# Kernel optimization log

Measured on AMD Instinct MI355X. Metric: run time of the kernel, lower is better.

Reference implementation:

```python
import jax, jax.numpy as jnp
import numpy as np

DIM = 192
HEADS = 4
HID = int(DIM * 2.66)  # 510, Restormer GDFN hidden dim
EPS_LN = 1e-6


def ln2d(x, w, b):
    # torch LayerNorm2d variant: global mean/std over (C,H,W), std is UNBIASED (ddof=1)
    n = x.shape[1] * x.shape[2] * x.shape[3]
    mean = x.mean(axis=(1, 2, 3), keepdims=True)
    var = ((x - mean) ** 2).sum(axis=(1, 2, 3), keepdims=True) / (n - 1)
    return (x - mean) / (jnp.sqrt(var) + EPS_LN) * w + b


def conv1x1(x, w):
    # w: [O, C]; pointwise conv as channel matmul
    return jnp.einsum('bchw,oc->bohw', x, w)


def dwconv3(x, w):
    # w: [C, 1, 3, 3] depthwise 3x3, padding=1
    return jax.lax.conv_general_dilated(
        x, w, window_strides=(1, 1), padding='SAME',
        dimension_numbers=('NCHW', 'OIHW', 'NCHW'),
        feature_group_count=x.shape[1])


def setup_inputs() -> dict:
    key = jax.random.key(0)
    ks = jax.random.split(key, 8)
    s = 0.02
    return {
        'x': jax.random.normal(ks[0], (2, DIM, 256, 256), dtype=jnp.float32),
        'n1_w': jnp.ones((1, DIM, 1, 1), jnp.float32),
        'n1_b': jnp.zeros((1, DIM, 1, 1), jnp.float32),
        'qkv_w': jax.random.normal(ks[1], (3 * DIM, DIM), jnp.float32) * s,
        'qkv_dw_w': jax.random.normal(ks[2], (3 * DIM, 1, 3, 3), jnp.float32) * s,
        'proj_w': jax.random.normal(ks[3], (DIM, DIM), jnp.float32) * s,
        'temperature': jnp.ones((HEADS, 1, 1), jnp.float32),
        'n2_w': jnp.ones((1, DIM, 1, 1), jnp.float32),
        'n2_b': jnp.zeros((1, DIM, 1, 1), jnp.float32),
        'ff_in_w': jax.random.normal(ks[4], (2 * HID, DIM), jnp.float32) * s,
        'ff_dw_w': jax.random.normal(ks[5], (2 * HID, 1, 3, 3), jnp.float32) * s,
        'ff_out_w': jax.random.normal(ks[6], (DIM, HID), jnp.float32) * s,
    }


def reference(x, n1_w, n1_b, qkv_w, qkv_dw_w, proj_w, temperature,
              n2_w, n2_b, ff_in_w, ff_dw_w, ff_out_w):
    b, c, h, w = x.shape
    hd = c // HEADS

    # ---- MDTA attention ----
    y = ln2d(x, n1_w, n1_b)
    qkv = dwconv3(conv1x1(y, qkv_w), qkv_dw_w)  # [b, 3c, h, w]
    q, k, v = jnp.split(qkv, 3, axis=1)
    q = q.reshape(b, HEADS, hd, h * w)
    k = k.reshape(b, HEADS, hd, h * w)
    v = v.reshape(b, HEADS, hd, h * w)
    # L2-normalize along spatial axis (F.normalize, eps=1e-12)
    q = q / jnp.maximum(jnp.linalg.norm(q, axis=-1, keepdims=True), 1e-12)
    k = k / jnp.maximum(jnp.linalg.norm(k, axis=-1, keepdims=True), 1e-12)
    attn = jnp.einsum('bhcn,bhdn->bhcd', q, k) * temperature  # [b,H,hd,hd]
    attn = jax.nn.softmax(attn, axis=-1)
    out = jnp.einsum('bhcd,bhdn->bhcn', attn, v).reshape(b, c, h, w)
    x = x + conv1x1(out, proj_w)

    # ---- GDFN feed-forward ----
    y = ln2d(x, n2_w, n2_b)
    y = dwconv3(conv1x1(y, ff_in_w), ff_dw_w)  # [b, 2*HID, h, w]
    x1, x2 = jnp.split(y, 2, axis=1)
    y = jax.nn.gelu(x1, approximate=False) * x2
    x = x + conv1x1(y, ff_out_w)
    return x
```

## Files before the change

### kernel.cpp

```cpp
#include <hip/hip_runtime.h>
#include <hip/hip_bf16.h>

typedef unsigned short u16;
typedef __attribute__((ext_vector_type(8))) short short8;
typedef __attribute__((ext_vector_type(8))) unsigned short ushort8v;
typedef __attribute__((ext_vector_type(4))) float f32x4;

#define NPIX  65536
#define HH    256
#define WW    256
#define BATCH 2
#define CDIM  192
#define NHEADS 4
#define HD    48
#define OQKV  576
#define HIDN  510
#define OPAD  1024
#define NSLOT 32

__device__ __forceinline__ float bf2f(u16 b) {
  union { unsigned u; float f; } v; v.u = ((unsigned)b) << 16; return v.f;
}
__device__ __forceinline__ u16 f2bf(float f) {
  __bf16 h = (__bf16)f;
  u16 r; __builtin_memcpy(&r, &h, 2); return r;
}
__device__ __forceinline__ void atomAddF(float* p, float v) { unsafeAtomicAdd(p, v); }
__device__ __forceinline__ void gload16(const void* g, void* l) {
  __builtin_amdgcn_global_load_lds((const __attribute__((address_space(1))) unsigned int*)g,
                                   (__attribute__((address_space(3))) unsigned int*)l, 16, 0, 0);
}
__device__ __forceinline__ void xcdswz(int& bx, int& by) {
  const int nx = gridDim.x;
  const int tot = nx * gridDim.y;
  const int lin = by * nx + bx;
  const int q = tot >> 3, r = tot & 7;
  const int xcd = lin & 7, pos = lin >> 3;
  const int nl = (xcd < r) ? (xcd * (q + 1) + pos) : (r * (q + 1) + (xcd - r) * q + pos);
  bx = nl % nx; by = nl / nx;
}
__device__ __forceinline__ void dw3row(const u16* __restrict__ rp, int jm, bool hasL, bool hasR,
                                       float w0, float w1, float w2, float* acc) {
  ushort8v m = *(const ushort8v*)(rp + jm);
  float f[10];
  f[0] = hasL ? bf2f(rp[jm - 1]) : 0.f;
  #pragma unroll
  for (int t = 0; t < 8; ++t) f[t + 1] = bf2f(m[t]);
  f[9] = hasR ? bf2f(rp[jm + 8]) : 0.f;
  #pragma unroll
  for (int i = 0; i < 8; ++i) acc[i] += w0 * f[i] + w1 * f[i + 1] + w2 * f[i + 2];
}

#define OFF_STATS1 ((size_t)0)
#define OFF_STATS2 ((size_t)512)
#define OFF_G      ((size_t)1024)
#define OFF_NQ     (OFF_G + 2359296)
#define OFF_NK     (OFF_NQ + 49152)
#define ZERO_BYTES (OFF_NK + 49152)
#define OFF_BQ     ZERO_BYTES
#define OFF_B2     (OFF_BQ + 4608)
#define OFF_M      (OFF_B2 + 8192)
#define OFF_WQ     (OFF_M + 294912)
#define OFF_W2B    (OFF_WQ + 442368)
#define OFF_W3     (OFF_W2B + 786432)
#define OFF_T      (OFF_W3 + 196608)
#define OFF_QKV    (OFF_T + 50331648)
#define OFF_BAND   (OFF_QKV + 150994944)

__global__ __launch_bounds__(256) void k_statsT(const float* __restrict__ P, u16* __restrict__ T,
                                                float* __restrict__ stats) {
  __shared__ u16 ld[128][200];
  const int b = blockIdx.y, n0 = blockIdx.x * 128, tid = threadIdx.x;
  const int slot = blockIdx.x & (NSLOT - 1);
  const float* Pb = P + (((size_t)b * CDIM) << 16) + n0;
  float s = 0.f, ss = 0.f;
  for (int it = 0; it < 24; ++it) {
    int idx = it * 256 + tid;
    int c = idx >> 5, j = idx & 31;
    float4 v = *(const float4*)(Pb + ((size_t)c << 16) + j * 4);
    s  += v.x + v.y + v.z + v.w;
    ss += v.x*v.x + v.y*v.y + v.z*v.z + v.w*v.w;
    int px = j * 4;
    ld[px][c] = f2bf(v.x); ld[px+1][c] = f2bf(v.y);
    ld[px+2][c] = f2bf(v.z); ld[px+3][c] = f2bf(v.w);
  }
  for (int off = 32; off; off >>= 1) { s += __shfl_down(s, off); ss += __shfl_down(ss, off); }
  __shared__ float ls[4], lss[4];
  const int wid = tid >> 6, lane = tid & 63;
  if (lane == 0) { ls[wid] = s; lss[wid] = ss; }
  __syncthreads();
  if (tid == 0) {
    atomAddF(&stats[(slot * BATCH + b) * 2 + 0], ls[0]+ls[1]+ls[2]+ls[3]);
    atomAddF(&stats[(slot * BATCH + b) * 2 + 1], lss[0]+lss[1]+lss[2]+lss[3]);
  }
  u16* Tb = T + (size_t)(b * NPIX + n0) * CDIM;
  for (int it = 0; it < 12; ++it) {
    int idx = it * 256 + tid;
    int ch = idx % 24, nl = idx / 24;
    union { u16 s[8]; uint4 v; } t;
    #pragma unroll
    for (int r = 0; r < 8; ++r) t.s[r] = ld[nl][ch * 8 + r];
    int sch = ch ^ (nl & 7);
    *(uint4*)((char*)(Tb + (size_t)nl * CDIM) + sch * 16) = t.v;
  }
}

__global__ void k_fold(const float* __restrict__ w_in, const float* __restrict__ ln_w,
                       const float* __restrict__ ln_b, const float* __restrict__ stats,
                       u16* __restrict__ W, float* __restrict__ bias, int O_real) {
  const int o = blockIdx.x, b = blockIdx.y, c = threadIdx.x;
  const int Mtot = gridDim.x;
  const float n = (float)(CDIM * NPIX);
  float sum = 0.f, sumsq = 0.f;
  for (int sl = 0; sl < NSLOT; ++sl) {
    sum   += stats[(sl * BATCH + b) * 2 + 0];
    sumsq += stats[(sl * BATCH + b) * 2 + 1];
  }
  const float mean = sum / n;
  const float var = (sumsq - sum * sum / n) / (n - 1.f);
  const float inv = 1.f / (sqrtf(var) + 1e-6f);
  float we = 0.f, cb = 0.f;
  if (o < O_real) {
    float wi = w_in[o * CDIM + c];
    float a  = ln_w[c] * inv;
    we = wi * a;
    cb = wi * (ln_b[c] - mean * a);
  }
  int sch = (c >> 3) ^ (o & 7);
  W[((size_t)b * Mtot + o) * CDIM + sch * 8 + (c & 7)] = f2bf(we);
  for (int off = 32; off; off >>= 1) cb += __shfl_down(cb, off);
  __shared__ float l[3];
  if ((threadIdx.x & 63) == 0) l[threadIdx.x >> 6] = cb;
  __syncthreads();
  if (threadIdx.x == 0) bias[b * Mtot + o] = l[0] + l[1] + l[2];
}

__global__ void k_fold3(const float* __restrict__ w, u16* __restrict__ W3) {
  const int o = blockIdx.x;
  for (int it = 0; it < 2; ++it) {
    int c = it * 256 + threadIdx.x;
    float v = (c < HIDN) ? w[o * HIDN + c] : 0.f;
    int sch = (c >> 3) ^ (o & 7);
    W3[o * 512 + sch * 8 + (c & 7)] = f2bf(v);
  }
}

template <int KTOT, int KC, int EPI, int STATS, int NT>
__global__ __launch_bounds__(256) void k_mgemm(
    const u16* __restrict__ Bm, const u16* __restrict__ Am,
    const float* __restrict__ bias,
    const u16* __restrict__ rT, long rTbstr,
    void* __restrict__ outv, long Obstr, int out_nstr,
    u16* __restrict__ tout, long toutbstr,
    int Mtot, long Bbstr, long Abstr,
    int nB_base, int nB_rows, int nO_base, float* __restrict__ stats)
{
  constexpr int RBC = KC * 2;
  constexpr int NFR = NT / 64;
  constexpr int LDSB = (NT + 64) * KC * 2;
  constexpr int EPIB = (EPI == 0) ? 64 * (NT + 8) * 2
                     : (EPI == 2) ? 128 * 66 * 4
                     : ((EPI == 3) ? 64 * 132 * 4 : 0);
  constexpr int TOT  = LDSB > EPIB ? LDSB : EPIB;
  __shared__ char lds[TOT];
  u16* lB = (u16*)lds;
  u16* lA = (u16*)(lds + NT * KC * 2);
  const int b = blockIdx.z;
  int bx = blockIdx.x, by = blockIdx.y;
  xcdswz(bx, by);
  const int o0 = bx * 64;
  const int nB = nB_base + by * NT;
  const int nO = nO_base + by * NT;
  const int tid = threadIdx.x;
  const int lane = tid & 63;
  const int wid = tid >> 6;

  if (EPI == 0 && (nB < 0 || nB >= nB_rows)) {
    u16* op = (u16*)outv;
    uint4 z; z.x = z.y = z.z = z.w = 0u;
    constexpr int CH8 = NT / 8;
    #pragma unroll
    for (int it = 0; it < NT / 32; ++it) {
      int idx = it * 256 + tid;
      int orow = idx / CH8, c8 = idx % CH8;
      *(uint4*)(op + (size_t)b * Obstr + (size_t)(o0 + orow) * out_nstr + nO + c8 * 8) = z;
    }
    return;
  }

  const u16* Bb = Bm + (size_t)b * Bbstr + (size_t)nB * KTOT;
  const u16* Ab = Am + (size_t)b * Abstr + (size_t)o0 * KTOT;

  f32x4 acc[4][NFR];
  #pragma unroll
  for (int m = 0; m < 4; ++m)
    #pragma unroll
    for (int nf = 0; nf < NFR; ++nf) acc[m][nf] = (f32x4){0.f, 0.f, 0.f, 0.f};

  for (int kc0 = 0; kc0 < KTOT; kc0 += KC) {
    if (kc0) __syncthreads();
    constexpr int NCH = KC / 8;
    #pragma unroll
    for (int it = 0; it < NT * NCH / 256; ++it) {
      int idx = it * 256 + tid; int r = idx / NCH, ch = idx % NCH;
      gload16((const char*)(Bb + (size_t)r * KTOT + kc0) + ch * 16, (char*)lB + idx * 16);
    }
    #pragma unroll
    for (int it = 0; it < 64 * NCH / 256; ++it) {
      int idx = it * 256 + tid; int r = idx / NCH, ch = idx % NCH;
      gload16((const char*)(Ab + (size_t)r * KTOT + kc0) + ch * 16, (char*)lA + idx * 16);
    }
    __syncthreads();
    const int lr = lane & 15, g = lane >> 4;
    #pragma unroll
    for (int ks = 0; ks < KC / 32; ++ks) {
      const int ck = ks * 4 + g;
      short8 afr[4], bfr[NFR];
      #pragma unroll
      for (int m = 0; m < 4; ++m) {
        int row = m * 16 + lr;
        afr[m] = *(const short8*)((const char*)lA + row * RBC + ((ck ^ (row & 7)) << 4));
      }
      #pragma unroll
      for (int nf = 0; nf < NFR; ++nf) {
        int row = wid * (NT / 4) + nf * 16 + lr;
        bfr[nf] = *(const short8*)((const char*)lB + row * RBC + ((ck ^ (row & 7)) << 4));
      }
      #pragma unroll
      for (int m = 0; m < 4; ++m)
        #pragma unroll
        for (int nf = 0; nf < NFR; ++nf)
          acc[m][nf] = __builtin_amdgcn_mfma_f32_16x16x32_bf16(afr[m], bfr[nf], acc[m][nf], 0, 0, 0);
    }
  }

  const int col = lane & 15, rg = lane >> 4;
  if constexpr (EPI == 0) {
    constexpr int NTP = NT + 8;
    u16* lst = (u16*)lds;
    __syncthreads();
    #pragma unroll
    for (int m = 0; m < 4; ++m)
      #pragma unroll
      for (int j = 0; j < 4; ++j) {
        int r = m * 16 + rg * 4 + j;
        float bv = bias[b * Mtot + o0 + r];
        #pragma unroll
        for (int nf = 0; nf < NFR; ++nf) {
          int nn = wid * (NT / 4) + nf * 16 + col;
          lst[r * NTP + nn] = f2bf(acc[m][nf][j] + bv);
        }
      }
    __syncthreads();
    u16* op = (u16*)outv;
    constexpr int CH8 = NT / 8;
    #pragma unroll
    for (int it = 0; it < 64 * CH8 / 256; ++it) {
      int idx = it * 256 + tid;
      int r = idx / CH8, ch = idx % CH8;
      uint4 v = *(const uint4*)(lst + r * NTP + ch * 8);
      *(uint4*)(op + (size_t)b * Obstr + (size_t)(o0 + r) * out_nstr + nO + ch * 8) = v;
    }
  } else if constexpr (EPI == 2) {
    float* lBf = (float*)lds;
    __syncthreads();
    #pragma unroll
    for (int m = 0; m < 4; ++m)
      #pragma unroll
      for (int nf = 0; nf < NFR; ++nf)
        #pragma unroll
        for (int j = 0; j < 4; ++j)
          lBf[(wid * 32 + nf * 16 + col) * 66 + m * 16 + rg * 4 + j] = acc[m][nf][j];
    __syncthreads();
    float s = 0.f, ss = 0.f;
    for (int it = 0; it < 4; ++it) {
      int idx = it * 256 + tid;
      int n = idx >> 3, ch3 = idx & 7;
      size_t rowoff = (size_t)(nO + n) * CDIM;
      int chunk = (o0 >> 3) + (ch3 ^ (n & 7));
      uint4 xv = *(const uint4*)((const char*)(rT + (size_t)b * rTbstr + rowoff) + chunk * 16);
      u16* xs = (u16*)&xv;
      union { u16 s[8]; uint4 v; } t;
      #pragma unroll
      for (int r = 0; r < 8; ++r) {
        float rv = bf2f(xs[r]) + lBf[n * 66 + ch3 * 8 + r];
        t.s[r] = f2bf(rv);
        if constexpr (STATS) { s += rv; ss += rv * rv; }
      }
      *(uint4*)((char*)(tout + (size_t)b * toutbstr + rowoff) + chunk * 16) = t.v;
    }
    if constexpr (STATS) {
      for (int off = 32; off; off >>= 1) { s += __shfl_down(s, off); ss += __shfl_down(ss, off); }
      __shared__ float sr1[4], sr2[4];
      if (lane == 0) { sr1[wid] = s; sr2[wid] = ss; }
      __syncthreads();
      if (tid == 0) {
        int slot = by & (NSLOT - 1);
        atomAddF(&stats[(slot * BATCH + b) * 2 + 0], sr1[0]+sr1[1]+sr1[2]+sr1[3]);
        atomAddF(&stats[(slot * BATCH + b) * 2 + 1], sr2[0]+sr2[1]+sr2[2]+sr2[3]);
      }
    }
  } else {
    u16* lAx = (u16*)lds;
    __syncthreads();
    for (int it = 0; it < 4; ++it) {
      int idx = it * 256 + tid;
      int n = idx >> 3, ch3 = idx & 7;
      int chunk = (o0 >> 3) + (ch3 ^ (n & 7));
      uint4 xv = *(const uint4*)((const char*)(rT + (size_t)b * rTbstr + (size_t)(nO + n) * CDIM) + chunk * 16);
      u16* xs = (u16*)&xv;
      #pragma unroll
      for (int r = 0; r < 8; ++r) lAx[n * 66 + ch3 * 8 + r] = xs[r];
    }
    __syncthreads();
    #pragma unroll
    for (int m = 0; m < 4; ++m)
      #pragma unroll
      for (int nf = 0; nf < NFR; ++nf)
        #pragma unroll
        for (int j = 0; j < 4; ++j) {
          int nl = wid * 32 + nf * 16 + col;
          acc[m][nf][j] += bf2f(lAx[nl * 66 + m * 16 + rg * 4 + j]);
        }
    __syncthreads();
    float* lstf = (float*)lds;
    #pragma unroll
    for (int m = 0; m < 4; ++m)
      #pragma unroll
      for (int nf = 0; nf < NFR; ++nf)
        #pragma unroll
        for (int j = 0; j < 4; ++j)
          lstf[(m * 16 + rg * 4 + j) * 132 + wid * 32 + nf * 16 + col] = acc[m][nf][j];
    __syncthreads();
    float* of = (float*)outv;
    #pragma unroll
    for (int it = 0; it < 8; ++it) {
      int idx = it * 256 + tid;
      int r = idx >> 5, q4 = idx & 31;
      float4 v = *(const float4*)&lstf[r * 132 + q4 * 4];
      *(float4*)(of + (size_t)b * Obstr + (size_t)(o0 + r) * out_nstr + nO + q4 * 4) = v;
    }
  }
}

__global__ __launch_bounds__(256) void k_gram(const u16* __restrict__ qkv,
                                              const float* __restrict__ dww,
                                              float* __restrict__ G,
                                              float* __restrict__ nq,
                                              float* __restrict__ nk) {
  __shared__ u16 qs[HD][128], ks2[HD][128];
  __shared__ u16 wq[HD][9], wk[HD][9];
  __shared__ float nql[HD], nkl[HD];
  int bx = blockIdx.x, by = blockIdx.y;
  xcdswz(bx, by);
  const int b = by >> 2, h = by & 3;
  const int row = bx >> 1, col0 = (bx & 1) * 128;
  const int slot = bx & (NSLOT - 1);
  const int bh = b * NHEADS + h;
  const int tid = threadIdx.x;

  for (int idx = tid; idx < HD * 9; idx += 256) {
    int c = idx / 9, k9 = idx % 9;
    wq[c][k9] = f2bf(dww[(h * HD + c) * 9 + k9]);
    wk[c][k9] = f2bf(dww[(CDIM + h * HD + c) * 9 + k9]);
  }
  __syncthreads();

  for (int it = 0; it < 6; ++it) {
    int idx = it * 256 + tid;
    int j = idx & 15, cz = idx >> 4;
    int c = cz % HD, qk = cz / HD;
    const u16* base = qkv + (((size_t)(b * OQKV + qk * CDIM + h * HD + c)) << 16);
    const u16* w = qk ? wk[c] : wq[c];
    float acc[8] = {0.f,0.f,0.f,0.f,0.f,0.f,0.f,0.f};
    const int jm = col0 + j * 8;
    const bool hasL = jm > 0, hasR = jm < 248;
    if (row > 0)   dw3row(base + (row - 1) * 256, jm, hasL, hasR, bf2f(w[0]), bf2f(w[1]), bf2f(w[2]), acc);
                   dw3row(base + row * 256,       jm, hasL, hasR, bf2f(w[3]), bf2f(w[4]), bf2f(w[5]), acc);
    if (row < 255) dw3row(base + (row + 1) * 256, jm, hasL, hasR, bf2f(w[6]), bf2f(w[7]), bf2f(w[8]), acc);
    union { u16 s[8]; ushort8v v; } rv;
    float sqs = 0.f;
    #pragma unroll
    for (int i = 0; i < 8; ++i) {
      rv.s[i] = f2bf(acc[i]);
      sqs += acc[i] * acc[i];
    }
    const int sw = (j ^ (c & 7)) * 8;
    if (qk) *(ushort8v*)&ks2[c][sw] = rv.v;
    else    *(ushort8v*)&qs[c][sw]  = rv.v;
    sqs += __shfl_down(sqs, 8);
    sqs += __shfl_down(sqs, 4);
    sqs += __shfl_down(sqs, 2);
    sqs += __shfl_down(sqs, 1);
    if ((tid & 15) == 0) { if (qk) nkl[c] = sqs; else nql[c] = sqs; }
  }
  __syncthreads();

  if (tid < HD) atomAddF(&nq[(slot * 2 * NHEADS + bh) * HD + tid], nql[tid]);
  else if (tid < 2*HD) atomAddF(&nk[(slot * 2 * NHEADS + bh) * HD + tid - HD], nkl[tid - HD]);

  const int lane = tid & 63, wid = tid >> 6;
  const int lr = lane & 15, g = lane >> 4;
  float* Gb = G + (size_t)(slot * 2 * NHEADS + bh) * HD * HD;
  for (int t = wid; t < 9; t += 4) {
    const int m = t / 3, nb = t % 3;
    f32x4 a4 = (f32x4){0.f, 0.f, 0.f, 0.f};
    #pragma unroll
    for (int ksi = 0; ksi < 4; ++ksi) {
      int ck = ksi * 4 + g;
      int ra = m * 16 + lr, rb = nb * 16 + lr;
      short8 af = *(const short8*)&qs[ra][(ck ^ (ra & 7)) * 8];
      short8 bf = *(const short8*)&ks2[rb][(ck ^ (rb & 7)) * 8];
      a4 = __builtin_amdgcn_mfma_f32_16x16x32_bf16(af, bf, a4, 0, 0, 0);
    }
    #pragma unroll
    for (int jj = 0; jj < 4; ++jj)
      atomAddF(&Gb[(m * 16 + g * 4 + jj) * HD + nb * 16 + lr], a4[jj]);
  }
}

__global__ void k_attnM(const float* __restrict__ G, const float* __restrict__ nq,
                        const float* __restrict__ nk, const float* __restrict__ temp,
                        const float* __restrict__ proj_w, u16* __restrict__ Mb16) {
  const int h = blockIdx.x, b = blockIdx.y;
  const int bh = b * NHEADS + h;
  __shared__ float at[HD][HD];
  __shared__ float nqs[HD], nks[HD];
  const int tid = threadIdx.x;
  if (tid < HD) {
    float s = 0.f;
    for (int sl = 0; sl < NSLOT; ++sl) s += nq[(sl * 2 * NHEADS + bh) * HD + tid];
    nqs[tid] = fmaxf(sqrtf(s), 1e-12f);
  } else if (tid >= 64 && tid < 64 + HD) {
    int c = tid - 64;
    float s = 0.f;
    for (int sl = 0; sl < NSLOT; ++sl) s += nk[(sl * 2 * NHEADS + bh) * HD + c];
    nks[c] = fmaxf(sqrtf(s), 1e-12f);
  }
  __syncthreads();
  const float t = temp[h];
  for (int idx = tid; idx < HD * HD; idx += 256) {
    int c = idx / HD, d = idx % HD;
    float g = 0.f;
    for (int sl = 0; sl < NSLOT; ++sl)
      g += G[(size_t)(sl * 2 * NHEADS + bh) * HD * HD + idx];
    at[c][d] = g / (nqs[c] * nks[d]) * t;
  }
  __syncthreads();
  if (tid < HD) {
    float m = -1e30f;
    for (int d = 0; d < HD; ++d) m = fmaxf(m, at[tid][d]);
    float s = 0.f;
    for (int d = 0; d < HD; ++d) { float e = __expf(at[tid][d] - m); at[tid][d] = e; s += e; }
    float inv = 1.f / s;
    for (int d = 0; d < HD; ++d) at[tid][d] *= inv;
  }
  __syncthreads();
  for (int idx = tid; idx < CDIM * HD; idx += 256) {
    int o = idx / HD, d = idx % HD;
    float acc = 0.f;
    for (int c = 0; c < HD; ++c) acc += proj_w[o * CDIM + h * HD + c] * at[c][d];
    int cf = h * HD + d;
    int sch = (cf >> 3) ^ (o & 7);
    Mb16[((size_t)(b * CDIM + o)) * CDIM + sch * 8 + (cf & 7)] = f2bf(acc);
  }
}

__global__ __launch_bounds__(256) void k_dwT(const u16* __restrict__ qkv,
                                             const float* __restrict__ dww,
                                             u16* __restrict__ vdwT, long vdwbstr) {
  __shared__ u16 ld[64][201];
  __shared__ float w9[CDIM][9];
  int bx = blockIdx.x, by = blockIdx.y;
  xcdswz(bx, by);
  const int b = by;
  const int p0 = bx * 64;
  const int row = p0 >> 8, col0 = p0 & 255;
  const int tid = threadIdx.x;
  for (int idx = tid; idx < CDIM * 9; idx += 256) w9[idx / 9][idx % 9] = dww[384 * 9 + idx];
  __syncthreads();
  for (int it = 0; it < 6; ++it) {
    int idx = it * 256 + tid;
    int j = idx & 7, c = idx >> 3;
    const u16* base = qkv + (((size_t)(b * OQKV + 384 + c)) << 16);
    const float* w = w9[c];
    float acc[8] = {0.f,0.f,0.f,0.f,0.f,0.f,0.f,0.f};
    const int jm = col0 + j * 8;
    const bool hasL = jm > 0, hasR = jm < 248;
    if (row > 0)   dw3row(base + (row - 1) * 256, jm, hasL, hasR, w[0], w[1], w[2], acc);
                   dw3row(base + row * 256,       jm, hasL, hasR, w[3], w[4], w[5], acc);
    if (row < 255) dw3row(base + (row + 1) * 256, jm, hasL, hasR, w[6], w[7], w[8], acc);
    #pragma unroll
    for (int i = 0; i < 8; ++i) ld[j * 8 + i][c] = f2bf(acc[i]);
  }
  __syncthreads();
  u16* Tb = vdwT + (size_t)b * vdwbstr + (size_t)p0 * CDIM;
  for (int it = 0; it < 6; ++it) {
    int idx = it * 256 + tid;
    int ch = idx % 24, pl = idx / 24;
    union { u16 s[8]; uint4 v; } t;
    #pragma unroll
    for (int r = 0; r < 8; ++r) t.s[r] = ld[pl][ch * 8 + r];
    int sch = ch ^ (pl & 7);
    *(uint4*)((char*)(Tb + (size_t)pl * CDIM) + sch * 16) = t.v;
  }
}

__global__ __launch_bounds__(256) void k_dwgT(const u16* __restrict__ hp_, const float* __restrict__ w9,
                                              u16* __restrict__ ygT, int rows_loc, int band_px) {
  __shared__ u16 ld[32][515];
  int bx = blockIdx.x, by = blockIdx.y;
  xcdswz(bx, by);
  const int b = by;
  const int p0 = bx * 32;
  const int olr = p0 >> 8, col0 = p0 & 255;
  const int tid = threadIdx.x;
  if (tid < 64) {
    int px = tid >> 1, c = 510 + (tid & 1);
    ld[px][c] = 0;
  }
  __syncthreads();
  for (int it = 0; it < 8; ++it) {
    int idx = it * 256 + tid;
    if (idx >= HIDN * 4) break;
    int j = idx & 3, c = idx >> 2;
    const u16* ia = hp_ + (size_t)(b * OPAD + c) * rows_loc * 256;
    const u16* ig = hp_ + (size_t)(b * OPAD + c + HIDN) * rows_loc * 256;
    float aa[8] = {0.f,0.f,0.f,0.f,0.f,0.f,0.f,0.f};
    float gg[8] = {0.f,0.f,0.f,0.f,0.f,0.f,0.f,0.f};
    const int jm = col0 + j * 8;
    const bool hasL = jm > 0, hasR = jm < 248;
    #pragma unroll
    for (int dr = 0; dr < 3; ++dr) {
      dw3row(ia + (olr + dr) * 256, jm, hasL, hasR,
             w9[c * 9 + dr * 3], w9[c * 9 + dr * 3 + 1], w9[c * 9 + dr * 3 + 2], aa);
      dw3row(ig + (olr + dr) * 256, jm, hasL, hasR,
             w9[(c + HIDN) * 9 + dr * 3], w9[(c + HIDN) * 9 + dr * 3 + 1],
             w9[(c + HIDN) * 9 + dr * 3 + 2], gg);
    }
    #pragma unroll
    for (int i = 0; i < 8; ++i) {
      float a = aa[i];
      float gel = 0.5f * a * (1.f + erff(a * 0.70710678118654752f));
      ld[j * 8 + i][c] = f2bf(gel * gg[i]);
    }
  }
  __syncthreads();
  u16* Tb = ygT + ((size_t)b * band_px + p0) * 512;
  for (int it = 0; it < 8; ++it) {
    int idx = it * 256 + tid;
    int ch = idx & 63, pl = idx >> 6;
    union { u16 s[8]; uint4 v; } t;
    #pragma unroll
    for (int r = 0; r < 8; ++r) t.s[r] = ld[pl][ch * 8 + r];
    int sch = ch ^ (pl & 7);
    *(uint4*)((char*)(Tb + (size_t)pl * 512) + sch * 16) = t.v;
  }
}

extern "C" void kernel_launch(void* const* d_in, const int* in_sizes, int n_in,
                              void* d_out, int out_size, void* d_ws, size_t ws_size,
                              hipStream_t stream) {
  const float* x       = (const float*)d_in[0];
  const float* n1_w    = (const float*)d_in[1];
  const float* n1_b    = (const float*)d_in[2];
  const float* qkv_w   = (const float*)d_in[3];
  const float* qkv_dw  = (const float*)d_in[4];
  const float* proj_w  = (const float*)d_in[5];
  const float* temp    = (const float*)d_in[6];
  const float* n2_w    = (const float*)d_in[7];
  const float* n2_b    = (const float*)d_in[8];
  const float* ff_in_w = (const float*)d_in[9];
  const float* ff_dw   = (const float*)d_in[10];
  const float* ff_out_w= (const float*)d_in[11];

  char* ws = (char*)d_ws;
  float* stats1 = (float*)(ws + OFF_STATS1);
  float* stats2 = (float*)(ws + OFF_STATS2);
  float* G      = (float*)(ws + OFF_G);
  float* nq     = (float*)(ws + OFF_NQ);
  float* nk     = (float*)(ws + OFF_NK);
  float* biasq  = (float*)(ws + OFF_BQ);
  float* bias2  = (float*)(ws + OFF_B2);
  u16*   Mb16   = (u16*)(ws + OFF_M);
  u16*   Wq     = (u16*)(ws + OFF_WQ);
  u16*   W2b    = (u16*)(ws + OFF_W2B);
  u16*   W3     = (u16*)(ws + OFF_W3);
  u16*   xT     = (u16*)(ws + OFF_T);
  u16*   qkv    = (u16*)(ws + OFF_QKV);
  u16*   vdwT   = qkv;
  u16*   x2T    = qkv + (size_t)CDIM * NPIX;
  const long qkvbstr = (long)OQKV * NPIX;
  float* outp   = (float*)d_out;

  int NP = 32;
  const int cand[4] = {2, 4, 8, 16};
  for (int i = 0; i < 4; ++i) {
    int rws = 256 / cand[i], rl = rws + 2;
    size_t band = (size_t)2 * OPAD * rl * 256 * 2 + (size_t)2 * rws * 256 * 512 * 2;
    if (OFF_BAND + band + ((size_t)8 << 20) <= ws_size) { NP = cand[i]; break; }
  }
  const int rows = 256 / NP, rows_loc = rows + 2, band_px = rows * 256;
  u16* hpre = (u16*)(ws + OFF_BAND);
  u16* ygT  = (u16*)(ws + OFF_BAND + (size_t)2 * OPAD * rows_loc * 256 * 2);

  hipMemsetAsync(ws, 0, ZERO_BYTES, stream);

  k_statsT<<<dim3(NPIX / 128, BATCH), 256, 0, stream>>>(x, xT, stats1);
  k_fold<<<dim3(OQKV, BATCH), CDIM, 0, stream>>>(qkv_w, n1_w, n1_b, stats1, Wq, biasq, OQKV);
  k_mgemm<192, 64, 0, 0, 256><<<dim3(OQKV / 64, NPIX / 256, BATCH), 256, 0, stream>>>(
      xT, Wq, biasq, nullptr, 0L, qkv, (long)OQKV * NPIX, NPIX, nullptr, 0L,
      OQKV, (long)NPIX * CDIM, (long)OQKV * CDIM, 0, NPIX, 0, nullptr);
  k_gram<<<dim3(512, BATCH * NHEADS), 256, 0, stream>>>(qkv, qkv_dw, G, nq, nk);
  k_attnM<<<dim3(NHEADS, BATCH), 256, 0, stream>>>(G, nq, nk, temp, proj_w, Mb16);
  k_dwT<<<dim3(NPIX / 64, BATCH), 256, 0, stream>>>(qkv, qkv_dw, vdwT, qkvbstr);
  k_mgemm<192, 64, 2, 1, 128><<<dim3(CDIM / 64, NPIX / 128, BATCH), 256, 0, stream>>>(
      vdwT, Mb16, nullptr, xT, (long)NPIX * CDIM, nullptr, 0L, 0, x2T, qkvbstr,
      CDIM, qkvbstr, (long)CDIM * CDIM, 0, NPIX, 0, stats2);

  k_fold<<<dim3(OPAD, BATCH), CDIM, 0, stream>>>(ff_in_w, n2_w, n2_b, stats2, W2b, bias2, 1020);
  k_fold3<<<dim3(CDIM), 256, 0, stream>>>(ff_out_w, W3);
  for (int rp = 0; rp < NP; ++rp) {
    const int band0 = rp * band_px;
    k_mgemm<192, 64, 0, 0, 256><<<dim3(OPAD / 64, rows_loc, BATCH), 256, 0, stream>>>(
        x2T, W2b, bias2, nullptr, 0L, hpre, (long)OPAD * rows_loc * 256, rows_loc * 256,
        nullptr, 0L, OPAD, qkvbstr, (long)OPAD * CDIM, band0 - 256, NPIX, 0, nullptr);
    k_dwgT<<<dim3(band_px / 32, BATCH), 256, 0, stream>>>(hpre, ff_dw, ygT, rows_loc, band_px);
    k_mgemm<512, 128, 3, 0, 128><<<dim3(CDIM / 64, rows * 2, BATCH), 256, 0, stream>>>(
        ygT, W3, nullptr, x2T, qkvbstr, outp, (long)CDIM * NPIX, NPIX, nullptr, 0L,
        CDIM, (long)band_px * 512, 0L, 0, band_px, band0, nullptr);
  }
}
```

Before: 756.2 us.

## Merge attention-matrix kernel into V depthwise kernel, add unroll hints, allow single band

The small k_attnM kernel is folded into k_dwT as extra blocks appended to the grid, reusing its shared memory, which removes one launch and the serialization gap between them. Partial unroll pragmas are added to the depthwise loops in gram, dwT and dwgT, and the dwgT loop break becomes a guarded body so it can unroll. The band-count search now tries NP=1 first, so with enough workspace the FFN runs as one large band with fewer launches but a bigger intermediate footprint. The xcdswz block swizzle is applied before the new attention-block check, which could misroute those extra blocks if the swizzle remaps indices.

```diff
diff --git a/kernel.cpp b/kernel.cpp
--- a/kernel.cpp
+++ b/kernel.cpp
@@ -366,6 +366,7 @@
   }
   __syncthreads();
 
+  #pragma unroll 2
   for (int it = 0; it < 6; ++it) {
     int idx = it * 256 + tid;
     int j = idx & 15, cz = idx >> 4;
@@ -419,66 +420,73 @@
   }
 }
 
-__global__ void k_attnM(const float* __restrict__ G, const float* __restrict__ nq,
-                        const float* __restrict__ nk, const float* __restrict__ temp,
-                        const float* __restrict__ proj_w, u16* __restrict__ Mb16) {
-  const int h = blockIdx.x, b = blockIdx.y;
-  const int bh = b * NHEADS + h;
-  __shared__ float at[HD][HD];
-  __shared__ float nqs[HD], nks[HD];
-  const int tid = threadIdx.x;
-  if (tid < HD) {
-    float s = 0.f;
-    for (int sl = 0; sl < NSLOT; ++sl) s += nq[(sl * 2 * NHEADS + bh) * HD + tid];
-    nqs[tid] = fmaxf(sqrtf(s), 1e-12f);
-  } else if (tid >= 64 && tid < 64 + HD) {
-    int c = tid - 64;
-    float s = 0.f;
-    for (int sl = 0; sl < NSLOT; ++sl) s += nk[(sl * 2 * NHEADS + bh) * HD + c];
-    nks[c] = fmaxf(sqrtf(s), 1e-12f);
-  }
-  __syncthreads();
-  const float t = temp[h];
-  for (int idx = tid; idx < HD * HD; idx += 256) {
-    int c = idx / HD, d = idx % HD;
-    float g = 0.f;
-    for (int sl = 0; sl < NSLOT; ++sl)
-      g += G[(size_t)(sl * 2 * NHEADS + bh) * HD * HD + idx];
-    at[c][d] = g / (nqs[c] * nks[d]) * t;
-  }
-  __syncthreads();
-  if (tid < HD) {
-    float m = -1e30f;
-    for (int d = 0; d < HD; ++d) m = fmaxf(m, at[tid][d]);
-    float s = 0.f;
-    for (int d = 0; d < HD; ++d) { float e = __expf(at[tid][d] - m); at[tid][d] = e; s += e; }
-    float inv = 1.f / s;
-    for (int d = 0; d < HD; ++d) at[tid][d] *= inv;
-  }
-  __syncthreads();
-  for (int idx = tid; idx < CDIM * HD; idx += 256) {
-    int o = idx / HD, d = idx % HD;
-    float acc = 0.f;
-    for (int c = 0; c < HD; ++c) acc += proj_w[o * CDIM + h * HD + c] * at[c][d];
-    int cf = h * HD + d;
-    int sch = (cf >> 3) ^ (o & 7);
-    Mb16[((size_t)(b * CDIM + o)) * CDIM + sch * 8 + (cf & 7)] = f2bf(acc);
-  }
-}
-
 __global__ __launch_bounds__(256) void k_dwT(const u16* __restrict__ qkv,
                                              const float* __restrict__ dww,
-                                             u16* __restrict__ vdwT, long vdwbstr) {
+                                             u16* __restrict__ vdwT, long vdwbstr,
+                                             const float* __restrict__ G,
+                                             const float* __restrict__ nq,
+                                             const float* __restrict__ nk,
+                                             const float* __restrict__ temp,
+                                             const float* __restrict__ proj_w,
+                                             u16* __restrict__ Mb16) {
   __shared__ u16 ld[64][201];
   __shared__ float w9[CDIM][9];
   int bx = blockIdx.x, by = blockIdx.y;
   xcdswz(bx, by);
   const int b = by;
+  const int tid = threadIdx.x;
+
+  if (bx >= NPIX / 64) {
+    const int h = bx - NPIX / 64;
+    const int bh = b * NHEADS + h;
+    float* atp = (float*)ld;
+    float* nqs = (float*)w9;
+    float* nks = nqs + 64;
+    if (tid < HD) {
+      float s = 0.f;
+      for (int sl = 0; sl < NSLOT; ++sl) s += nq[(sl * 2 * NHEADS + bh) * HD + tid];
+      nqs[tid] = fmaxf(sqrtf(s), 1e-12f);
+    } else if (tid >= 64 && tid < 64 + HD) {
+      int c = tid - 64;
+      float s = 0.f;
+      for (int sl = 0; sl < NSLOT; ++sl) s += nk[(sl * 2 * NHEADS + bh) * HD + c];
+      nks[c] = fmaxf(sqrtf(s), 1e-12f);
+    }
+    __syncthreads();
+    const float t = temp[h];
+    for (int idx = tid; idx < HD * HD; idx += 256) {
+      int c = idx / HD, d = idx % HD;
+      float g = 0.f;
+      for (int sl = 0; sl < NSLOT; ++sl)
+        g += G[(size_t)(sl * 2 * NHEADS + bh) * HD * HD + idx];
+      atp[idx] = g / (nqs[c] * nks[d]) * t;
+    }
+    __syncthreads();
+    if (tid < HD) {
+      float m = -1e30f;
+      for (int d = 0; d < HD; ++d) m = fmaxf(m, atp[tid * HD + d]);
+      float s = 0.f;
+      for (int d = 0; d < HD; ++d) { float e = __expf(atp[tid * HD + d] - m); atp[tid * HD + d] = e; s += e; }
+      float inv = 1.f / s;
+      for (int d = 0; d < HD; ++d) atp[tid * HD + d] *= inv;
+    }
+    __syncthreads();
+    for (int idx = tid; idx < CDIM * HD; idx += 256) {
+      int o = idx / HD, d = idx % HD;
+      float acc = 0.f;
+      for (int c = 0; c < HD; ++c) acc += proj_w[o * CDIM + h * HD + c] * atp[c * HD + d];
+      int cf = h * HD + d;
+      int sch = (cf >> 3) ^ (o & 7);
+      Mb16[((size_t)(b * CDIM + o)) * CDIM + sch * 8 + (cf & 7)] = f2bf(acc);
+    }
+    return;
+  }
+
   const int p0 = bx * 64;
   const int row = p0 >> 8, col0 = p0 & 255;
-  const int tid = threadIdx.x;
   for (int idx = tid; idx < CDIM * 9; idx += 256) w9[idx / 9][idx % 9] = dww[384 * 9 + idx];
   __syncthreads();
+  #pragma unroll 2
   for (int it = 0; it < 6; ++it) {
     int idx = it * 256 + tid;
     int j = idx & 7, c = idx >> 3;
@@ -520,29 +528,31 @@
     ld[px][c] = 0;
   }
   __syncthreads();
+  #pragma unroll 2
   for (int it = 0; it < 8; ++it) {
     int idx = it * 256 + tid;
-    if (idx >= HIDN * 4) break;
-    int j = idx & 3, c = idx >> 2;
-    const u16* ia = hp_ + (size_t)(b * OPAD + c) * rows_loc * 256;
-    const u16* ig = hp_ + (size_t)(b * OPAD + c + HIDN) * rows_loc * 256;
-    float aa[8] = {0.f,0.f,0.f,0.f,0.f,0.f,0.f,0.f};
-    float gg[8] = {0.f,0.f,0.f,0.f,0.f,0.f,0.f,0.f};
-    const int jm = col0 + j * 8;
-    const bool hasL = jm > 0, hasR = jm < 248;
-    #pragma unroll
-    for (int dr = 0; dr < 3; ++dr) {
-      dw3row(ia + (olr + dr) * 256, jm, hasL, hasR,
-             w9[c * 9 + dr * 3], w9[c * 9 + dr * 3 + 1], w9[c * 9 + dr * 3 + 2], aa);
-      dw3row(ig + (olr + dr) * 256, jm, hasL, hasR,
-             w9[(c + HIDN) * 9 + dr * 3], w9[(c + HIDN) * 9 + dr * 3 + 1],
-             w9[(c + HIDN) * 9 + dr * 3 + 2], gg);
-    }
-    #pragma unroll
-    for (int i = 0; i < 8; ++i) {
-      float a = aa[i];
-      float gel = 0.5f * a * (1.f + erff(a * 0.70710678118654752f));
-      ld[j * 8 + i][c] = f2bf(gel * gg[i]);
+    if (idx < HIDN * 4) {
+      int j = idx & 3, c = idx >> 2;
+      const u16* ia = hp_ + (size_t)(b * OPAD + c) * rows_loc * 256;
+      const u16* ig = hp_ + (size_t)(b * OPAD + c + HIDN) * rows_loc * 256;
+      float aa[8] = {0.f,0.f,0.f,0.f,0.f,0.f,0.f,0.f};
+      float gg[8] = {0.f,0.f,0.f,0.f,0.f,0.f,0.f,0.f};
+      const int jm = col0 + j * 8;
+      const bool hasL = jm > 0, hasR = jm < 248;
+      #pragma unroll
+      for (int dr = 0; dr < 3; ++dr) {
+        dw3row(ia + (olr + dr) * 256, jm, hasL, hasR,
+               w9[c * 9 + dr * 3], w9[c * 9 + dr * 3 + 1], w9[c * 9 + dr * 3 + 2], aa);
+        dw3row(ig + (olr + dr) * 256, jm, hasL, hasR,
+               w9[(c + HIDN) * 9 + dr * 3], w9[(c + HIDN) * 9 + dr * 3 + 1],
+               w9[(c + HIDN) * 9 + dr * 3 + 2], gg);
+      }
+      #pragma unroll
+      for (int i = 0; i < 8; ++i) {
+        float a = aa[i];
+        float gel = 0.5f * a * (1.f + erff(a * 0.70710678118654752f));
+        ld[j * 8 + i][c] = f2bf(gel * gg[i]);
+      }
     }
   }
   __syncthreads();
@@ -594,8 +604,8 @@
   float* outp   = (float*)d_out;
 
   int NP = 32;
-  const int cand[4] = {2, 4, 8, 16};
-  for (int i = 0; i < 4; ++i) {
+  const int cand[5] = {1, 2, 4, 8, 16};
+  for (int i = 0; i < 5; ++i) {
     int rws = 256 / cand[i], rl = rws + 2;
     size_t band = (size_t)2 * OPAD * rl * 256 * 2 + (size_t)2 * rws * 256 * 512 * 2;
     if (OFF_BAND + band + ((size_t)8 << 20) <= ws_size) { NP = cand[i]; break; }
@@ -612,8 +622,8 @@
       xT, Wq, biasq, nullptr, 0L, qkv, (long)OQKV * NPIX, NPIX, nullptr, 0L,
       OQKV, (long)NPIX * CDIM, (long)OQKV * CDIM, 0, NPIX, 0, nullptr);
   k_gram<<<dim3(512, BATCH * NHEADS), 256, 0, stream>>>(qkv, qkv_dw, G, nq, nk);
-  k_attnM<<<dim3(NHEADS, BATCH), 256, 0, stream>>>(G, nq, nk, temp, proj_w, Mb16);
-  k_dwT<<<dim3(NPIX / 64, BATCH), 256, 0, stream>>>(qkv, qkv_dw, vdwT, qkvbstr);
+  k_dwT<<<dim3(NPIX / 64 + NHEADS, BATCH), 256, 0, stream>>>(
+      qkv, qkv_dw, vdwT, qkvbstr, G, nq, nk, temp, proj_w, Mb16);
   k_mgemm<192, 64, 2, 1, 128><<<dim3(CDIM / 64, NPIX / 128, BATCH), 256, 0, stream>>>(
       vdwT, Mb16, nullptr, xT, (long)NPIX * CDIM, nullptr, 0L, 0, x2T, qkvbstr,
       CDIM, qkvbstr, (long)CDIM * CDIM, 0, NPIX, 0, stats2);
```

Result: no change. 748.3 us, median of 2 (-1.0%).
